# Kernel tuning notes

Hardware: AMD Instinct MI355X
Metric: run time of the kernel (lower is better)

The kernel has to match this reference:

```python
import jax, jax.numpy as jnp
import numpy as np

N_NODES = 200000
N_EDGES = 6400000
IN_F, HID, OUT = 28, 16, 2


def setup_inputs() -> dict:
    key = jax.random.key(0)
    k1, k2, k3, k4 = jax.random.split(key, 4)
    x = jax.random.normal(k1, (N_NODES, IN_F), dtype=jnp.float32)
    edge_index = jax.random.randint(k2, (2, N_EDGES), 0, N_NODES, dtype=jnp.int64)
    # Glorot-ish init for the two GCNConv weights
    W1 = jax.random.normal(k3, (IN_F, HID), dtype=jnp.float32) / np.sqrt(IN_F)
    b1 = jnp.zeros((HID,), dtype=jnp.float32)
    W2 = jax.random.normal(k4, (HID, OUT), dtype=jnp.float32) / np.sqrt(HID)
    b2 = jnp.zeros((OUT,), dtype=jnp.float32)
    return {"x": x, "edge_index": edge_index, "W1": W1, "b1": b1, "W2": W2, "b2": b2}


def _gcn_conv(h, W, b, src, dst, n_nodes):
    # PyG GCNConv: h' = D^{-1/2} (A + I) D^{-1/2} (h W) + b, self-loops already in src/dst
    h = h @ W  # [N, F_out] — transform first (small F), then aggregate
    deg = jax.ops.segment_sum(jnp.ones_like(dst, dtype=h.dtype), dst, num_segments=n_nodes)
    dis = jnp.where(deg > 0, jax.lax.rsqrt(jnp.maximum(deg, 1.0)), 0.0)
    norm = dis[src] * dis[dst]                    # [E]
    msg = h[src] * norm[:, None]                  # gather + scale
    agg = jax.ops.segment_sum(msg, dst, num_segments=n_nodes)  # scatter-add
    return agg + b


def reference(x, edge_index, W1, b1, W2, b2):
    n = x.shape[0]
    loops = jnp.arange(n, dtype=edge_index.dtype)
    src = jnp.concatenate([edge_index[0], loops])  # add self-loops
    dst = jnp.concatenate([edge_index[1], loops])
    h = _gcn_conv(x, W1, b1, src, dst, n)
    h = jax.nn.relu(h)
    # F.dropout(training=self.training): inference mode -> identity
    h = _gcn_conv(h, W2, b2, src, dst, n)
    return jax.nn.log_softmax(h, axis=1)
```

## Files before the change

### kernel.cpp

```cpp
#include <hip/hip_runtime.h>
#include <hip/hip_fp16.h>
#include <math.h>

#define N_IN_F 28
#define N_HID 16
#define NPB 256
#define NBK 1024
#define EPB 8192
#define SRC_BITS 18
#define SRC_MASK ((1 << SRC_BITS) - 1)
#define STAGE_CAP 10240


__global__ void __launch_bounds__(512)
k_bhist(const int* __restrict__ dst, unsigned short* __restrict__ chunk_hist, int ne) {
    __shared__ int hist[NBK];
    int tid = threadIdx.x;
    for (int t = tid; t < NBK; t += 512) hist[t] = 0;
    __syncthreads();
    int e0 = blockIdx.x * EPB;
    int e1 = min(e0 + EPB, ne);
    for (int e = e0 + tid; e < e1; e += 512) atomicAdd(&hist[dst[e] >> 8], 1);
    __syncthreads();
    unsigned short* ch = chunk_hist + (size_t)blockIdx.x * NBK;
    for (int t = tid; t < NBK; t += 512) ch[t] = (unsigned short)hist[t];
}

__global__ void __launch_bounds__(256)
k_colscan(const unsigned short* __restrict__ chunk_hist, int* __restrict__ gdelta,
          int* __restrict__ total, int nchunk) {
    __shared__ int p[16][17];
    int tid = threadIdx.x;
    int j = tid & 15;
    int g = tid >> 4;
    int bkt = blockIdx.x * 16 + j;
    int cpg = (nchunk + 15) >> 4;
    int c0 = g * cpg, c1 = min(c0 + cpg, nchunk);

    int s = 0;
    for (int c = c0; c < c1; ++c) s += chunk_hist[(size_t)c * NBK + bkt];
    p[g][j] = s;
    __syncthreads();

    if (tid < 16) {
        int run = 0;
#pragma unroll
        for (int gg = 0; gg < 16; ++gg) { int t = p[gg][tid]; p[gg][tid] = run; run += t; }
        total[blockIdx.x * 16 + tid] = run;
    }
    __syncthreads();

    int run = p[g][j];
    for (int c = c0; c < c1; ++c) {
        int h = chunk_hist[(size_t)c * NBK + bkt];
        gdelta[(size_t)c * NBK + bkt] = run;
        run += h;
    }
}

__global__ void k_top(const int* __restrict__ total, int* __restrict__ base, int ne) {
    __shared__ int sm[NBK];
    int tid = threadIdx.x;
    int v = total[tid];
    sm[tid] = v;
    __syncthreads();
    for (int off = 1; off < NBK; off <<= 1) {
        int t = (tid >= off) ? sm[tid - off] : 0;
        __syncthreads();
        sm[tid] += t;
        __syncthreads();
    }
    base[tid] = sm[tid] - v;
    if (tid == 0) base[NBK] = ne;
}

__global__ void __launch_bounds__(1024)
k_bin(const int* __restrict__ src, const int* __restrict__ dst,
      const unsigned short* __restrict__ chunk_hist, const int* __restrict__ gdelta,
      const int* __restrict__ base, int* __restrict__ binned, int ne) {
    __shared__ int gpos[NBK];
    __shared__ int lcur[NBK];
    __shared__ int wpart[16];
    __shared__ int stage[EPB];
    __shared__ unsigned short sbid[EPB];
    int tid = threadIdx.x;
    int lane = tid & 63;
    int wid = tid >> 6;
    int chunk = blockIdx.x;

    int h = chunk_hist[(size_t)chunk * NBK + tid];
    int val = h;
#pragma unroll
    for (int off = 1; off < 64; off <<= 1) {
        int t = __shfl_up(val, off, 64);
        if (lane >= off) val += t;
    }
    if (lane == 63) wpart[wid] = val;
    __syncthreads();
    if (wid == 0) {
        int p = (lane < 16) ? wpart[lane] : 0;
#pragma unroll
        for (int off = 1; off < 16; off <<= 1) {
            int t = __shfl_up(p, off, 64);
            if (lane >= off) p += t;
        }
        if (lane < 16) wpart[lane] = p;
    }
    __syncthreads();
    int wbase = (wid > 0) ? wpart[wid - 1] : 0;
    int excl = wbase + val - h;
    gpos[tid] = base[tid] + gdelta[(size_t)chunk * NBK + tid] - excl;
    lcur[tid] = excl;
    __syncthreads();

    int e0 = chunk * EPB;
    int csz = min(EPB, ne - e0);

    for (int i = tid; i < csz; i += 1024) {
        int d = dst[e0 + i];
        int b = d >> 8;
        int r = atomicAdd(&lcur[b], 1);
        stage[r] = src[e0 + i] | ((d & (NPB - 1)) << SRC_BITS);
        sbid[r] = (unsigned short)b;
    }
    __syncthreads();

    for (int i = tid; i < csz; i += 1024) {
        binned[gpos[sbid[i]] + i] = stage[i];
    }
}

__global__ void __launch_bounds__(512)
k_sort2(const int* __restrict__ base, const int* __restrict__ binned,
        int* __restrict__ binned2, int* __restrict__ row_start,
        float* __restrict__ dis, const float* __restrict__ x,
        const float* __restrict__ W1, __half* __restrict__ hs1,
        int n, int nb_total) {
    __shared__ int cnt[NPB];
    __shared__ int pos[NPB];
    __shared__ int cur[NPB];
    __shared__ float w[N_IN_F * N_HID];
    __shared__ int stage[STAGE_CAP];
    int tid = threadIdx.x;
    if (tid < NPB) cnt[tid] = 0;
    for (int t = tid; t < N_IN_F * N_HID; t += 512) w[t] = W1[t];
    __syncthreads();

    int b = blockIdx.x;
    int e0 = base[b], e1 = base[b + 1];
    int csz = e1 - e0;

    for (int e = e0 + tid; e < e1; e += 512) atomicAdd(&cnt[binned[e] >> SRC_BITS], 1);
    __syncthreads();

    int v = (tid < NPB) ? cnt[tid] : 0;
    if (tid < NPB) pos[tid] = v;
    __syncthreads();
    for (int off = 1; off < NPB; off <<= 1) {
        int t = (tid < NPB && tid >= off) ? pos[tid - off] : 0;
        __syncthreads();
        if (tid < NPB) pos[tid] += t;
        __syncthreads();
    }
    if (tid < NPB) {
        int excl = pos[tid] - v;
        cur[tid] = excl;
        int g = b * NPB + tid;
        if (g < n) {
            row_start[g] = e0 + excl;
            dis[g] = rsqrtf((float)(v + 1));
        }
    }
    if (b == nb_total - 1 && tid == 0) row_start[n] = e1;
    __syncthreads();

    for (int e = e0 + tid; e < e1; e += 512) {
        int p = binned[e];
        int r = atomicAdd(&cur[p >> SRC_BITS], 1);
        int val = p & SRC_MASK;
        if (r < STAGE_CAP) stage[r] = val;
        else binned2[e0 + r] = val;
    }
    __syncthreads();

    int lim = min(csz, STAGE_CAP);
    for (int i = tid; i < lim; i += 512) binned2[e0 + i] = stage[i];

    if (tid < NPB) {
        int g = b * NPB + tid;
        if (g < n) {
            float di = rsqrtf((float)(cnt[tid] + 1));
            float xi[N_IN_F];
            const float4* xr = (const float4*)(x + (size_t)g * N_IN_F);
#pragma unroll
            for (int q = 0; q < N_IN_F / 4; ++q) {
                float4 vv = xr[q];
                xi[4 * q + 0] = vv.x; xi[4 * q + 1] = vv.y;
                xi[4 * q + 2] = vv.z; xi[4 * q + 3] = vv.w;
            }
            __half2 hp[N_HID / 2];
#pragma unroll
            for (int f2 = 0; f2 < N_HID / 2; ++f2) {
                float ha = 0.0f, hb = 0.0f;
#pragma unroll
                for (int k = 0; k < N_IN_F; ++k) {
                    ha = fmaf(xi[k], w[k * N_HID + 2 * f2], ha);
                    hb = fmaf(xi[k], w[k * N_HID + 2 * f2 + 1], hb);
                }
                hp[f2] = __floats2half2_rn(ha * di, hb * di);
            }
            int4* dstp = (int4*)(hs1 + (size_t)g * N_HID);
            dstp[0] = *(const int4*)&hp[0];
            dstp[1] = *(const int4*)&hp[4];
        }
    }
}


__global__ void __launch_bounds__(256)
k_agg1(const int* __restrict__ row_start, const int* __restrict__ esrc,
       const __half2* __restrict__ hs1, const float* __restrict__ dis,
       const float* __restrict__ b1, const float* __restrict__ W2,
       float2* __restrict__ hs2, int n) {
    int t = blockIdx.x * blockDim.x + threadIdx.x;
    int node = t >> 3;
    int f2 = t & 7;
    if (node >= n) return;

    int beg = row_start[node];
    int end = row_start[node + 1];
    const __half2* H = hs1 + f2;

    float2 sl = __half22float2(H[node * 8]);
    float ax = sl.x, ay = sl.y;
    float a0x = 0.f, a0y = 0.f, a1x = 0.f, a1y = 0.f;
    float a2x = 0.f, a2y = 0.f, a3x = 0.f, a3y = 0.f;
    int j = beg;
    for (; j + 16 <= end; j += 16) {
        int s[16];
#pragma unroll
        for (int q = 0; q < 16; ++q) s[q] = esrc[j + q];
        float2 v[16];
#pragma unroll
        for (int q = 0; q < 16; ++q) v[q] = __half22float2(H[s[q] * 8]);
#pragma unroll
        for (int q = 0; q < 16; q += 4) {
            a0x += v[q + 0].x; a0y += v[q + 0].y;
            a1x += v[q + 1].x; a1y += v[q + 1].y;
            a2x += v[q + 2].x; a2y += v[q + 2].y;
            a3x += v[q + 3].x; a3y += v[q + 3].y;
        }
    }
    for (; j + 4 <= end; j += 4) {
        int s0 = esrc[j], s1 = esrc[j + 1], s2 = esrc[j + 2], s3 = esrc[j + 3];
        float2 v0 = __half22float2(H[s0 * 8]);
        float2 v1 = __half22float2(H[s1 * 8]);
        float2 v2 = __half22float2(H[s2 * 8]);
        float2 v3 = __half22float2(H[s3 * 8]);
        a0x += v0.x; a0y += v0.y; a1x += v1.x; a1y += v1.y;
        a2x += v2.x; a2y += v2.y; a3x += v3.x; a3y += v3.y;
    }
    for (; j < end; ++j) {
        float2 v0 = __half22float2(H[esrc[j] * 8]);
        ax += v0.x; ay += v0.y;
    }
    ax += (a0x + a1x) + (a2x + a3x);
    ay += (a0y + a1y) + (a2y + a3y);

    float di = dis[node];
    float vx = fmaxf(fmaf(di, ax, b1[2 * f2 + 0]), 0.0f);
    float vy = fmaxf(fmaf(di, ay, b1[2 * f2 + 1]), 0.0f);
    float c0 = vx * W2[4 * f2 + 0] + vy * W2[4 * f2 + 2];
    float c1 = vx * W2[4 * f2 + 1] + vy * W2[4 * f2 + 3];
#pragma unroll
    for (int off = 4; off > 0; off >>= 1) {
        c0 += __shfl_xor(c0, off, 8);
        c1 += __shfl_xor(c1, off, 8);
    }
    if (f2 == 0) {
        float2 o;
        o.x = c0 * di;
        o.y = c1 * di;
        hs2[node] = o;
    }
}

__global__ void __launch_bounds__(256)
k_agg2(const int* __restrict__ row_start, const int* __restrict__ esrc,
       const float2* __restrict__ hs2, const float* __restrict__ dis,
       const float* __restrict__ b2, float2* __restrict__ out, int n) {
    int t = blockIdx.x * blockDim.x + threadIdx.x;
    int node = t >> 2;
    int l = t & 3;
    if (node >= n) return;

    int beg = row_start[node];
    int end = row_start[node + 1];
    float cx = 0.f, cy = 0.f, dx = 0.f, dy = 0.f;
    int j = beg + l;
    for (; j + 4 < end; j += 8) {
        int s0 = esrc[j];
        int s1 = esrc[j + 4];
        float2 v0 = hs2[s0];
        float2 v1 = hs2[s1];
        cx += v0.x; cy += v0.y;
        dx += v1.x; dy += v1.y;
    }
    if (j < end) {
        float2 v = hs2[esrc[j]];
        cx += v.x; cy += v.y;
    }
    cx += dx; cy += dy;
#pragma unroll
    for (int off = 2; off > 0; off >>= 1) {
        cx += __shfl_xor(cx, off, 4);
        cy += __shfl_xor(cy, off, 4);
    }
    if (l == 0) {
        float2 self = hs2[node];
        float di = dis[node];
        float a = fmaf(di, cx + self.x, b2[0]);
        float c = fmaf(di, cy + self.y, b2[1]);
        float m = fmaxf(a, c);
        float lse = m + logf(expf(a - m) + expf(c - m));
        float2 o;
        o.x = a - lse;
        o.y = c - lse;
        out[node] = o;
    }
}


extern "C" void kernel_launch(void* const* d_in, const int* in_sizes, int n_in,
                              void* d_out, int out_size, void* d_ws, size_t ws_size,
                              hipStream_t stream) {
    const float* x  = (const float*)d_in[0];
    const int*   ei = (const int*)d_in[1];
    const float* W1 = (const float*)d_in[2];
    const float* b1 = (const float*)d_in[3];
    const float* W2 = (const float*)d_in[4];
    const float* b2 = (const float*)d_in[5];
    float2* out = (float2*)d_out;

    const int n  = in_sizes[0] / N_IN_F;
    const int ne = in_sizes[1] / 2;
    const int* src = ei;
    const int* dst = ei + ne;
    const int nb = (n + NPB - 1) / NPB;
    const int nchunk = (ne + EPB - 1) / EPB;

    int* ws_i = (int*)d_ws;
    int* total     = ws_i;
    int* base      = total + 1024;
    int* row_start = base + 1028;
    float* dis     = (float*)(row_start + n + 4);
    float2* hs2    = (float2*)(dis + n);
    __half* hs1    = (__half*)(hs2 + n);
    unsigned short* chunk_hist = (unsigned short*)((int*)hs1 + 8 * (size_t)n);
    int* binned2   = (int*)chunk_hist + ((size_t)nchunk * NBK + 1) / 2;
    int* binned    = binned2 + ne;
    int* gdelta    = binned2;

    const int B = 256;

    k_bhist<<<dim3(nchunk), dim3(512), 0, stream>>>(dst, chunk_hist, ne);
    k_colscan<<<dim3(NBK / 16), dim3(B), 0, stream>>>(chunk_hist, gdelta, total, nchunk);
    k_top<<<dim3(1), dim3(NBK), 0, stream>>>(total, base, ne);
    k_bin<<<dim3(nchunk), dim3(1024), 0, stream>>>(src, dst, chunk_hist, gdelta, base, binned, ne);
    k_sort2<<<dim3(nb), dim3(512), 0, stream>>>(base, binned, binned2, row_start, dis,
                                                x, W1, hs1, n, nb);
    {
        long long tot = (long long)n * 8;
        k_agg1<<<dim3((unsigned)((tot + B - 1) / B)), dim3(B), 0, stream>>>(
            row_start, binned2, (const __half2*)hs1, dis, b1, W2, hs2, n);
    }
    {
        long long tot = (long long)n * 4;
        k_agg2<<<dim3((unsigned)((tot + B - 1) / B)), dim3(B), 0, stream>>>(
            row_start, binned2, hs2, dis, b2, out, n);
    }
}
```

Measured before the change: 181.5 us.

## Split layer-1 aggregation into two source-range passes for cache locality

```diff
diff --git a/kernel.cpp b/kernel.cpp
--- a/kernel.cpp
+++ b/kernel.cpp
@@ -133,16 +133,16 @@
 __global__ void __launch_bounds__(512)
 k_sort2(const int* __restrict__ base, const int* __restrict__ binned,
         int* __restrict__ binned2, int* __restrict__ row_start,
-        float* __restrict__ dis, const float* __restrict__ x,
-        const float* __restrict__ W1, __half* __restrict__ hs1,
-        int n, int nb_total) {
-    __shared__ int cnt[NPB];
-    __shared__ int pos[NPB];
-    __shared__ int cur[NPB];
+        int* __restrict__ mid, float* __restrict__ dis,
+        const float* __restrict__ x, const float* __restrict__ W1,
+        __half* __restrict__ hs1, int n, int nhalf, int nb_total) {
+    __shared__ int cnt[2 * NPB];
+    __shared__ int pos[2 * NPB];
+    __shared__ int cur[2 * NPB];
     __shared__ float w[N_IN_F * N_HID];
     __shared__ int stage[STAGE_CAP];
     int tid = threadIdx.x;
-    if (tid < NPB) cnt[tid] = 0;
+    cnt[tid] = 0;
     for (int t = tid; t < N_IN_F * N_HID; t += 512) w[t] = W1[t];
     __syncthreads();
 
@@ -150,36 +150,47 @@
     int e0 = base[b], e1 = base[b + 1];
     int csz = e1 - e0;
 
-    for (int e = e0 + tid; e < e1; e += 512) atomicAdd(&cnt[binned[e] >> SRC_BITS], 1);
-    __syncthreads();
-
-    int v = (tid < NPB) ? cnt[tid] : 0;
-    if (tid < NPB) pos[tid] = v;
-    __syncthreads();
-    for (int off = 1; off < NPB; off <<= 1) {
-        int t = (tid < NPB && tid >= off) ? pos[tid - off] : 0;
-        __syncthreads();
-        if (tid < NPB) pos[tid] += t;
-        __syncthreads();
-    }
-    if (tid < NPB) {
-        int excl = pos[tid] - v;
-        cur[tid] = excl;
-        int g = b * NPB + tid;
-        if (g < n) {
-            row_start[g] = e0 + excl;
-            dis[g] = rsqrtf((float)(v + 1));
-        }
-    }
-    if (b == nb_total - 1 && tid == 0) row_start[n] = e1;
-    __syncthreads();
-
     for (int e = e0 + tid; e < e1; e += 512) {
         int p = binned[e];
-        int r = atomicAdd(&cur[p >> SRC_BITS], 1);
-        int val = p & SRC_MASK;
-        if (r < STAGE_CAP) stage[r] = val;
-        else binned2[e0 + r] = val;
+        int s = p & SRC_MASK;
+        int key = ((p >> SRC_BITS) << 1) | (s >= nhalf ? 1 : 0);
+        atomicAdd(&cnt[key], 1);
+    }
+    __syncthreads();
+
+    int v = cnt[tid];
+    pos[tid] = v;
+    __syncthreads();
+    for (int off = 1; off < 2 * NPB; off <<= 1) {
+        int t = (tid >= off) ? pos[tid - off] : 0;
+        __syncthreads();
+        pos[tid] += t;
+        __syncthreads();
+    }
+    cur[tid] = pos[tid] - v;
+    float di_reg = 0.0f;
+    if (tid < NPB) {
+        int g = b * NPB + tid;
+        int lo = cnt[2 * tid], hi = cnt[2 * tid + 1];
+        int exlo = pos[2 * tid] - lo;
+        int exhi = pos[2 * tid + 1] - hi;
+        di_reg = rsqrtf((float)(lo + hi + 1));
+        if (g < n) {
+            row_start[g] = e0 + exlo;
+            mid[g] = e0 + exhi;
+            dis[g] = di_reg;
+        }
+    }
+    if (b == nb_total - 1 && tid == 0) row_start[n] = e1;
+    __syncthreads();
+
+    for (int e = e0 + tid; e < e1; e += 512) {
+        int p = binned[e];
+        int s = p & SRC_MASK;
+        int key = ((p >> SRC_BITS) << 1) | (s >= nhalf ? 1 : 0);
+        int r = atomicAdd(&cur[key], 1);
+        if (r < STAGE_CAP) stage[r] = s;
+        else binned2[e0 + r] = s;
     }
     __syncthreads();
 
@@ -189,7 +200,6 @@
     if (tid < NPB) {
         int g = b * NPB + tid;
         if (g < n) {
-            float di = rsqrtf((float)(cnt[tid] + 1));
             float xi[N_IN_F];
             const float4* xr = (const float4*)(x + (size_t)g * N_IN_F);
 #pragma unroll
@@ -207,7 +217,7 @@
                     ha = fmaf(xi[k], w[k * N_HID + 2 * f2], ha);
                     hb = fmaf(xi[k], w[k * N_HID + 2 * f2 + 1], hb);
                 }
-                hp[f2] = __floats2half2_rn(ha * di, hb * di);
+                hp[f2] = __floats2half2_rn(ha * di_reg, hb * di_reg);
             }
             int4* dstp = (int4*)(hs1 + (size_t)g * N_HID);
             dstp[0] = *(const int4*)&hp[0];
@@ -217,71 +227,103 @@
 }
 
 
+template <int HALF>
 __global__ void __launch_bounds__(256)
-k_agg1(const int* __restrict__ row_start, const int* __restrict__ esrc,
-       const __half2* __restrict__ hs1, const float* __restrict__ dis,
-       const float* __restrict__ b1, const float* __restrict__ W2,
+k_agg1(const int* __restrict__ row_start, const int* __restrict__ mid,
+       const int* __restrict__ esrc, const uint2* __restrict__ hs1,
+       const float* __restrict__ dis, const float* __restrict__ b1,
+       const float* __restrict__ W2, uint2* __restrict__ part,
        float2* __restrict__ hs2, int n) {
     int t = blockIdx.x * blockDim.x + threadIdx.x;
-    int node = t >> 3;
-    int f2 = t & 7;
+    int node = t >> 2;
+    int f4 = t & 3;
     if (node >= n) return;
 
-    int beg = row_start[node];
-    int end = row_start[node + 1];
-    const __half2* H = hs1 + f2;
-
-    float2 sl = __half22float2(H[node * 8]);
-    float ax = sl.x, ay = sl.y;
-    float a0x = 0.f, a0y = 0.f, a1x = 0.f, a1y = 0.f;
-    float a2x = 0.f, a2y = 0.f, a3x = 0.f, a3y = 0.f;
+    int beg, end;
+    if (HALF == 0) { beg = row_start[node]; end = mid[node]; }
+    else           { beg = mid[node];       end = row_start[node + 1]; }
+
+    const uint2* H = hs1 + f4;
+
+    float a0, a1, a2, a3;
+    if (HALF == 0) {
+        uint2 u = H[(size_t)node * 4];
+        float2 f0 = __half22float2(*(const __half2*)&u.x);
+        float2 f1 = __half22float2(*(const __half2*)&u.y);
+        a0 = f0.x; a1 = f0.y; a2 = f1.x; a3 = f1.y;
+    } else {
+        uint2 u = part[(size_t)node * 4 + f4];
+        float2 f0 = __half22float2(*(const __half2*)&u.x);
+        float2 f1 = __half22float2(*(const __half2*)&u.y);
+        a0 = f0.x; a1 = f0.y; a2 = f1.x; a3 = f1.y;
+    }
+
     int j = beg;
-    for (; j + 16 <= end; j += 16) {
-        int s[16];
-#pragma unroll
-        for (int q = 0; q < 16; ++q) s[q] = esrc[j + q];
-        float2 v[16];
-#pragma unroll
-        for (int q = 0; q < 16; ++q) v[q] = __half22float2(H[s[q] * 8]);
-#pragma unroll
-        for (int q = 0; q < 16; q += 4) {
-            a0x += v[q + 0].x; a0y += v[q + 0].y;
-            a1x += v[q + 1].x; a1y += v[q + 1].y;
-            a2x += v[q + 2].x; a2y += v[q + 2].y;
-            a3x += v[q + 3].x; a3y += v[q + 3].y;
+    for (; j + 8 <= end; j += 8) {
+        int s[8];
+#pragma unroll
+        for (int q = 0; q < 8; ++q) s[q] = __builtin_nontemporal_load(&esrc[j + q]);
+        uint2 u[8];
+#pragma unroll
+        for (int q = 0; q < 8; ++q) u[q] = H[(size_t)s[q] * 4];
+#pragma unroll
+        for (int q = 0; q < 8; ++q) {
+            float2 f0 = __half22float2(*(const __half2*)&u[q].x);
+            float2 f1 = __half22float2(*(const __half2*)&u[q].y);
+            a0 += f0.x; a1 += f0.y; a2 += f1.x; a3 += f1.y;
         }
     }
     for (; j + 4 <= end; j += 4) {
-        int s0 = esrc[j], s1 = esrc[j + 1], s2 = esrc[j + 2], s3 = esrc[j + 3];
-        float2 v0 = __half22float2(H[s0 * 8]);
-        float2 v1 = __half22float2(H[s1 * 8]);
-        float2 v2 = __half22float2(H[s2 * 8]);
-        float2 v3 = __half22float2(H[s3 * 8]);
-        a0x += v0.x; a0y += v0.y; a1x += v1.x; a1y += v1.y;
-        a2x += v2.x; a2y += v2.y; a3x += v3.x; a3y += v3.y;
+        int s[4];
+#pragma unroll
+        for (int q = 0; q < 4; ++q) s[q] = __builtin_nontemporal_load(&esrc[j + q]);
+        uint2 u[4];
+#pragma unroll
+        for (int q = 0; q < 4; ++q) u[q] = H[(size_t)s[q] * 4];
+#pragma unroll
+        for (int q = 0; q < 4; ++q) {
+            float2 f0 = __half22float2(*(const __half2*)&u[q].x);
+            float2 f1 = __half22float2(*(const __half2*)&u[q].y);
+            a0 += f0.x; a1 += f0.y; a2 += f1.x; a3 += f1.y;
+        }
     }
     for (; j < end; ++j) {
-        float2 v0 = __half22float2(H[esrc[j] * 8]);
-        ax += v0.x; ay += v0.y;
-    }
-    ax += (a0x + a1x) + (a2x + a3x);
-    ay += (a0y + a1y) + (a2y + a3y);
-
-    float di = dis[node];
-    float vx = fmaxf(fmaf(di, ax, b1[2 * f2 + 0]), 0.0f);
-    float vy = fmaxf(fmaf(di, ay, b1[2 * f2 + 1]), 0.0f);
-    float c0 = vx * W2[4 * f2 + 0] + vy * W2[4 * f2 + 2];
-    float c1 = vx * W2[4 * f2 + 1] + vy * W2[4 * f2 + 3];
-#pragma unroll
-    for (int off = 4; off > 0; off >>= 1) {
-        c0 += __shfl_xor(c0, off, 8);
-        c1 += __shfl_xor(c1, off, 8);
-    }
-    if (f2 == 0) {
-        float2 o;
-        o.x = c0 * di;
-        o.y = c1 * di;
-        hs2[node] = o;
+        int s0 = __builtin_nontemporal_load(&esrc[j]);
+        uint2 u = H[(size_t)s0 * 4];
+        float2 f0 = __half22float2(*(const __half2*)&u.x);
+        float2 f1 = __half22float2(*(const __half2*)&u.y);
+        a0 += f0.x; a1 += f0.y; a2 += f1.x; a3 += f1.y;
+    }
+
+    if (HALF == 0) {
+        __half2 p0 = __floats2half2_rn(a0, a1);
+        __half2 p1 = __floats2half2_rn(a2, a3);
+        uint2 o;
+        o.x = *(const unsigned*)&p0;
+        o.y = *(const unsigned*)&p1;
+        part[(size_t)node * 4 + f4] = o;
+    } else {
+        float di = dis[node];
+        int f = 4 * f4;
+        float v0 = fmaxf(fmaf(di, a0, b1[f + 0]), 0.0f);
+        float v1 = fmaxf(fmaf(di, a1, b1[f + 1]), 0.0f);
+        float v2 = fmaxf(fmaf(di, a2, b1[f + 2]), 0.0f);
+        float v3 = fmaxf(fmaf(di, a3, b1[f + 3]), 0.0f);
+        float c0 = v0 * W2[2 * f + 0] + v1 * W2[2 * f + 2]
+                 + v2 * W2[2 * f + 4] + v3 * W2[2 * f + 6];
+        float c1 = v0 * W2[2 * f + 1] + v1 * W2[2 * f + 3]
+                 + v2 * W2[2 * f + 5] + v3 * W2[2 * f + 7];
+#pragma unroll
+        for (int off = 2; off > 0; off >>= 1) {
+            c0 += __shfl_xor(c0, off, 4);
+            c1 += __shfl_xor(c1, off, 4);
+        }
+        if (f4 == 0) {
+            float2 o;
+            o.x = c0 * di;
+            o.y = c1 * di;
+            hs2[node] = o;
+        }
     }
 }
 
@@ -299,15 +341,15 @@
     float cx = 0.f, cy = 0.f, dx = 0.f, dy = 0.f;
     int j = beg + l;
     for (; j + 4 < end; j += 8) {
-        int s0 = esrc[j];
-        int s1 = esrc[j + 4];
+        int s0 = __builtin_nontemporal_load(&esrc[j]);
+        int s1 = __builtin_nontemporal_load(&esrc[j + 4]);
         float2 v0 = hs2[s0];
         float2 v1 = hs2[s1];
         cx += v0.x; cy += v0.y;
         dx += v1.x; dy += v1.y;
     }
     if (j < end) {
-        float2 v = hs2[esrc[j]];
+        float2 v = hs2[__builtin_nontemporal_load(&esrc[j])];
         cx += v.x; cy += v.y;
     }
     cx += dx; cy += dy;
@@ -348,6 +390,7 @@
     const int* dst = ei + ne;
     const int nb = (n + NPB - 1) / NPB;
     const int nchunk = (ne + EPB - 1) / EPB;
+    const int nhalf = n / 2;
 
     int* ws_i = (int*)d_ws;
     int* total     = ws_i;
@@ -360,6 +403,8 @@
     int* binned2   = (int*)chunk_hist + ((size_t)nchunk * NBK + 1) / 2;
     int* binned    = binned2 + ne;
     int* gdelta    = binned2;
+    int* mid       = (int*)chunk_hist;
+    uint2* part    = (uint2*)binned;
 
     const int B = 256;
 
@@ -367,16 +412,16 @@
     k_colscan<<<dim3(NBK / 16), dim3(B), 0, stream>>>(chunk_hist, gdelta, total, nchunk);
     k_top<<<dim3(1), dim3(NBK), 0, stream>>>(total, base, ne);
     k_bin<<<dim3(nchunk), dim3(1024), 0, stream>>>(src, dst, chunk_hist, gdelta, base, binned, ne);
-    k_sort2<<<dim3(nb), dim3(512), 0, stream>>>(base, binned, binned2, row_start, dis,
-                                                x, W1, hs1, n, nb);
-    {
-        long long tot = (long long)n * 8;
-        k_agg1<<<dim3((unsigned)((tot + B - 1) / B)), dim3(B), 0, stream>>>(
-            row_start, binned2, (const __half2*)hs1, dis, b1, W2, hs2, n);
-    }
+    k_sort2<<<dim3(nb), dim3(512), 0, stream>>>(base, binned, binned2, row_start, mid, dis,
+                                                x, W1, hs1, n, nhalf, nb);
     {
         long long tot = (long long)n * 4;
-        k_agg2<<<dim3((unsigned)((tot + B - 1) / B)), dim3(B), 0, stream>>>(
+        unsigned nbk = (unsigned)((tot + B - 1) / B);
+        k_agg1<0><<<dim3(nbk), dim3(B), 0, stream>>>(
+            row_start, mid, binned2, (const uint2*)hs1, dis, b1, W2, part, hs2, n);
+        k_agg1<1><<<dim3(nbk), dim3(B), 0, stream>>>(
+            row_start, mid, binned2, (const uint2*)hs1, dis, b1, W2, part, hs2, n);
+        k_agg2<<<dim3(nbk), dim3(B), 0, stream>>>(
             row_start, binned2, hs2, dis, b2, out, n);
     }
 }
```

Measured after the change: 220.2 us. 1.21x slower.

## Sub-sort edges by source slice within each dst row; unroll agg2 gathers

Applied to the files above, without the earlier changes.

```diff
diff --git a/kernel.cpp b/kernel.cpp
--- a/kernel.cpp
+++ b/kernel.cpp
@@ -10,6 +10,8 @@
 #define SRC_BITS 18
 #define SRC_MASK ((1 << SRC_BITS) - 1)
 #define STAGE_CAP 10240
+#define NSL 16
+#define SL_SHIFT 14
 
 
 __global__ void __launch_bounds__(512)
@@ -136,13 +138,13 @@
         float* __restrict__ dis, const float* __restrict__ x,
         const float* __restrict__ W1, __half* __restrict__ hs1,
         int n, int nb_total) {
-    __shared__ int cnt[NPB];
-    __shared__ int pos[NPB];
-    __shared__ int cur[NPB];
+    __shared__ int cnt[NPB * NSL];
+    __shared__ int cur[NPB * NSL];
+    __shared__ int ps[512];
     __shared__ float w[N_IN_F * N_HID];
     __shared__ int stage[STAGE_CAP];
     int tid = threadIdx.x;
-    if (tid < NPB) cnt[tid] = 0;
+    for (int t = tid; t < NPB * NSL; t += 512) cnt[t] = 0;
     for (int t = tid; t < N_IN_F * N_HID; t += 512) w[t] = W1[t];
     __syncthreads();
 
@@ -150,36 +152,52 @@
     int e0 = base[b], e1 = base[b + 1];
     int csz = e1 - e0;
 
-    for (int e = e0 + tid; e < e1; e += 512) atomicAdd(&cnt[binned[e] >> SRC_BITS], 1);
-    __syncthreads();
-
-    int v = (tid < NPB) ? cnt[tid] : 0;
-    if (tid < NPB) pos[tid] = v;
-    __syncthreads();
-    for (int off = 1; off < NPB; off <<= 1) {
-        int t = (tid < NPB && tid >= off) ? pos[tid - off] : 0;
-        __syncthreads();
-        if (tid < NPB) pos[tid] += t;
-        __syncthreads();
-    }
-    if (tid < NPB) {
-        int excl = pos[tid] - v;
-        cur[tid] = excl;
-        int g = b * NPB + tid;
-        if (g < n) {
-            row_start[g] = e0 + excl;
-            dis[g] = rsqrtf((float)(v + 1));
-        }
-    }
-    if (b == nb_total - 1 && tid == 0) row_start[n] = e1;
-    __syncthreads();
-
     for (int e = e0 + tid; e < e1; e += 512) {
         int p = binned[e];
-        int r = atomicAdd(&cur[p >> SRC_BITS], 1);
-        int val = p & SRC_MASK;
-        if (r < STAGE_CAP) stage[r] = val;
-        else binned2[e0 + r] = val;
+        int key = ((p >> SRC_BITS) << 4) | ((p & SRC_MASK) >> SL_SHIFT);
+        atomicAdd(&cnt[key], 1);
+    }
+    __syncthreads();
+
+    int c[8];
+    int sum = 0;
+#pragma unroll
+    for (int q = 0; q < 8; ++q) { c[q] = cnt[8 * tid + q]; sum += c[q]; }
+    ps[tid] = sum;
+    __syncthreads();
+    for (int off = 1; off < 512; off <<= 1) {
+        int t = (tid >= off) ? ps[tid - off] : 0;
+        __syncthreads();
+        ps[tid] += t;
+        __syncthreads();
+    }
+    int run = ps[tid] - sum;
+#pragma unroll
+    for (int q = 0; q < 8; ++q) { cur[8 * tid + q] = run; run += c[q]; }
+    __syncthreads();
+
+    float di_reg = 0.0f;
+    if (tid < NPB) {
+        int g = b * NPB + tid;
+        int deg = 0;
+#pragma unroll
+        for (int q = 0; q < NSL; ++q) deg += cnt[tid * NSL + q];
+        di_reg = rsqrtf((float)(deg + 1));
+        if (g < n) {
+            row_start[g] = e0 + cur[tid * NSL];
+            dis[g] = di_reg;
+        }
+    }
+    if (b == nb_total - 1 && tid == 0) row_start[n] = e1;
+    __syncthreads();
+
+    for (int e = e0 + tid; e < e1; e += 512) {
+        int p = binned[e];
+        int s = p & SRC_MASK;
+        int key = ((p >> SRC_BITS) << 4) | (s >> SL_SHIFT);
+        int r = atomicAdd(&cur[key], 1);
+        if (r < STAGE_CAP) stage[r] = s;
+        else binned2[e0 + r] = s;
     }
     __syncthreads();
 
@@ -189,7 +207,6 @@
     if (tid < NPB) {
         int g = b * NPB + tid;
         if (g < n) {
-            float di = rsqrtf((float)(cnt[tid] + 1));
             float xi[N_IN_F];
             const float4* xr = (const float4*)(x + (size_t)g * N_IN_F);
 #pragma unroll
@@ -207,7 +224,7 @@
                     ha = fmaf(xi[k], w[k * N_HID + 2 * f2], ha);
                     hb = fmaf(xi[k], w[k * N_HID + 2 * f2 + 1], hb);
                 }
-                hp[f2] = __floats2half2_rn(ha * di, hb * di);
+                hp[f2] = __floats2half2_rn(ha * di_reg, hb * di_reg);
             }
             int4* dstp = (int4*)(hs1 + (size_t)g * N_HID);
             dstp[0] = *(const int4*)&hp[0];
@@ -296,21 +313,22 @@
 
     int beg = row_start[node];
     int end = row_start[node + 1];
-    float cx = 0.f, cy = 0.f, dx = 0.f, dy = 0.f;
+    float cx = 0.f, cy = 0.f;
     int j = beg + l;
-    for (; j + 4 < end; j += 8) {
-        int s0 = esrc[j];
-        int s1 = esrc[j + 4];
-        float2 v0 = hs2[s0];
-        float2 v1 = hs2[s1];
-        cx += v0.x; cy += v0.y;
-        dx += v1.x; dy += v1.y;
-    }
-    if (j < end) {
+    for (; j + 28 < end; j += 32) {
+        int s[8];
+#pragma unroll
+        for (int q = 0; q < 8; ++q) s[q] = esrc[j + 4 * q];
+        float2 v[8];
+#pragma unroll
+        for (int q = 0; q < 8; ++q) v[q] = hs2[s[q]];
+#pragma unroll
+        for (int q = 0; q < 8; ++q) { cx += v[q].x; cy += v[q].y; }
+    }
+    for (; j < end; j += 4) {
         float2 v = hs2[esrc[j]];
         cx += v.x; cy += v.y;
     }
-    cx += dx; cy += dy;
 #pragma unroll
     for (int off = 2; off > 0; off >>= 1) {
         cx += __shfl_xor(cx, off, 4);
```

New measurement: 199.6 us. 1.1x slower.
